# Performance work log

Hardware: AMD Instinct MI355X
Metric: run time of the kernel (lower is better)

Reference implementation:

```python
import jax, jax.numpy as jnp
import numpy as np


def poly_feature(x, degree):
    """Monomial feature expansion along channel dim, exactly matching the
    original index-tracking loop order. x: [B, n, H, W] -> [B, F, H, W]."""
    n = x.shape[1]
    feature = [x]
    index = list(range(n))
    for _d in range(1, degree):
        new = []
        k = 0
        for i in range(n):
            term = x[:, i:i + 1] * feature[-1][:, index[i]:]
            new.append(term)
            index[i] = k
            k = k + term.shape[1]
        feature.append(jnp.concatenate(new, axis=1))
    return jnp.concatenate(feature, axis=1)


def setup_inputs() -> dict:
    key = jax.random.key(0)
    k1, k2, k3 = jax.random.split(key, 3)
    B, C, H, W = 16, 3, 512, 512
    degree = 3
    F = 19  # monomials of degree 1..3 in 3 vars: 3 + 6 + 10
    x = jax.random.uniform(k1, (B, C, H, W), dtype=jnp.float32)
    weight = jax.random.normal(k2, (F, C), dtype=jnp.float32)
    bias = jax.random.normal(k3, (C,), dtype=jnp.float32)
    return {"x": x, "weight": weight, "bias": bias, "degree": degree}


def reference(x, weight, bias, degree):
    # f: [B, F, H, W]; linear map over feature dim -> [B, 3, H, W]
    f = poly_feature(x, degree)
    pred = jnp.einsum("bfhw,fc->bchw", f, weight) + bias[None, :, None, None]
    return pred
```

## Files before the change

### kernel.cpp

```cpp
#include <hip/hip_runtime.h>


constexpr int HW = 512 * 512;
constexpr int LOG2_HW = 18;

typedef float v4f __attribute__((ext_vector_type(4)));

__device__ __forceinline__ float rfl(float v) {
    return __uint_as_float(__builtin_amdgcn_readfirstlane(__float_as_uint(v)));
}

__global__ __launch_bounds__(256) void ct_kernel(
    const float* __restrict__ x, const float* __restrict__ wgt,
    const float* __restrict__ bias, float* __restrict__ out, int ngroups)
{
    float w[57];
#pragma unroll
    for (int i = 0; i < 57; ++i) w[i] = rfl(wgt[i]);
    const float b0 = rfl(bias[0]);
    const float b1 = rfl(bias[1]);
    const float b2 = rfl(bias[2]);

    const int g = blockIdx.x * blockDim.x + threadIdx.x;
    if (g >= ngroups) return;

    const int p  = g << 2;
    const int b  = p >> LOG2_HW;
    const int hw = p & (HW - 1);

    const float* base = x + (size_t)b * 3 * HW + hw;
    v4f v0 = __builtin_nontemporal_load(reinterpret_cast<const v4f*>(base));
    v4f v1 = __builtin_nontemporal_load(reinterpret_cast<const v4f*>(base + HW));
    v4f v2 = __builtin_nontemporal_load(reinterpret_cast<const v4f*>(base + 2 * HW));

    v4f o0, o1, o2;
#pragma unroll
    for (int j = 0; j < 4; ++j) {
        const float a = v0[j], bch = v1[j], c = v2[j];
        float f[19];
        f[0]  = a;          f[1]  = bch;        f[2]  = c;
        f[3]  = a * a;      f[4]  = a * bch;    f[5]  = a * c;
        f[6]  = bch * bch;  f[7]  = bch * c;    f[8]  = c * c;
        f[9]  = a * f[3];   f[10] = a * f[4];   f[11] = a * f[5];
        f[12] = a * f[6];   f[13] = a * f[7];   f[14] = a * f[8];
        f[15] = bch * f[6]; f[16] = bch * f[7]; f[17] = bch * f[8];
        f[18] = c * f[8];

        float s0 = b0, s1 = b1, s2 = b2;
#pragma unroll
        for (int k = 0; k < 19; ++k) {
            s0 = fmaf(f[k], w[3 * k + 0], s0);
            s1 = fmaf(f[k], w[3 * k + 1], s1);
            s2 = fmaf(f[k], w[3 * k + 2], s2);
        }
        o0[j] = s0; o1[j] = s1; o2[j] = s2;
    }

    float* obase = out + (size_t)b * 3 * HW + hw;
    __builtin_nontemporal_store(o0, reinterpret_cast<v4f*>(obase));
    __builtin_nontemporal_store(o1, reinterpret_cast<v4f*>(obase + HW));
    __builtin_nontemporal_store(o2, reinterpret_cast<v4f*>(obase + 2 * HW));
}

extern "C" void kernel_launch(void* const* d_in, const int* in_sizes, int n_in,
                              void* d_out, int out_size, void* d_ws, size_t ws_size,
                              hipStream_t stream) {
    const float* x    = (const float*)d_in[0];
    const float* wgt  = (const float*)d_in[1];
    const float* bias = (const float*)d_in[2];
    float* out = (float*)d_out;

    const int npix    = in_sizes[0] / 3;
    const int ngroups = npix / 4;
    const int block   = 256;
    const int grid    = (ngroups + block - 1) / block;
    ct_kernel<<<grid, block, 0, stream>>>(x, wgt, bias, out, ngroups);
}
```

Measured before the change: 24.13 us.

## Use grid-stride persistent loop with register prefetch of next group

Replaces the one-group-per-thread launch with a fixed grid of 1024 blocks that stride over all pixel groups, loading the next group's three channel vectors into registers before computing the current one. The goal is to overlap global-load latency with the polynomial FMAs and to amortise the weight and bias uniform loads across several groups. It also switches the nontemporal loads and stores to plain ones, which changes cache behaviour. The trade-offs are a fixed grid size and higher register pressure from the prefetched vectors.

```diff
diff --git a/kernel.cpp b/kernel.cpp
--- a/kernel.cpp
+++ b/kernel.cpp
@@ -8,6 +8,13 @@
 
 __device__ __forceinline__ float rfl(float v) {
     return __uint_as_float(__builtin_amdgcn_readfirstlane(__float_as_uint(v)));
+}
+
+__device__ __forceinline__ const float* group_base(const float* x, int g) {
+    const int p  = g << 2;
+    const int b  = p >> LOG2_HW;
+    const int hw = p & (HW - 1);
+    return x + (size_t)b * 3 * HW + hw;
 }
 
 __global__ __launch_bounds__(256) void ct_kernel(
@@ -21,45 +28,62 @@
     const float b1 = rfl(bias[1]);
     const float b2 = rfl(bias[2]);
 
-    const int g = blockIdx.x * blockDim.x + threadIdx.x;
+    const int nthreads = gridDim.x * blockDim.x;
+    int g = blockIdx.x * blockDim.x + threadIdx.x;
     if (g >= ngroups) return;
 
-    const int p  = g << 2;
-    const int b  = p >> LOG2_HW;
-    const int hw = p & (HW - 1);
+    const float* base = group_base(x, g);
+    v4f va = *reinterpret_cast<const v4f*>(base);
+    v4f vb = *reinterpret_cast<const v4f*>(base + HW);
+    v4f vc = *reinterpret_cast<const v4f*>(base + 2 * HW);
 
-    const float* base = x + (size_t)b * 3 * HW + hw;
-    v4f v0 = __builtin_nontemporal_load(reinterpret_cast<const v4f*>(base));
-    v4f v1 = __builtin_nontemporal_load(reinterpret_cast<const v4f*>(base + HW));
-    v4f v2 = __builtin_nontemporal_load(reinterpret_cast<const v4f*>(base + 2 * HW));
+    for (;;) {
+        const int gn = g + nthreads;
+        const bool has_next = gn < ngroups;
+        v4f na, nb, nc;
+        if (has_next) {
+            const float* nbase = group_base(x, gn);
+            na = *reinterpret_cast<const v4f*>(nbase);
+            nb = *reinterpret_cast<const v4f*>(nbase + HW);
+            nc = *reinterpret_cast<const v4f*>(nbase + 2 * HW);
+        }
 
-    v4f o0, o1, o2;
+        v4f o0, o1, o2;
 #pragma unroll
-    for (int j = 0; j < 4; ++j) {
-        const float a = v0[j], bch = v1[j], c = v2[j];
-        float f[19];
-        f[0]  = a;          f[1]  = bch;        f[2]  = c;
-        f[3]  = a * a;      f[4]  = a * bch;    f[5]  = a * c;
-        f[6]  = bch * bch;  f[7]  = bch * c;    f[8]  = c * c;
-        f[9]  = a * f[3];   f[10] = a * f[4];   f[11] = a * f[5];
-        f[12] = a * f[6];   f[13] = a * f[7];   f[14] = a * f[8];
-        f[15] = bch * f[6]; f[16] = bch * f[7]; f[17] = bch * f[8];
-        f[18] = c * f[8];
+        for (int j = 0; j < 4; ++j) {
+            const float a = va[j], bch = vb[j], c = vc[j];
+            float f[19];
+            f[0]  = a;          f[1]  = bch;        f[2]  = c;
+            f[3]  = a * a;      f[4]  = a * bch;    f[5]  = a * c;
+            f[6]  = bch * bch;  f[7]  = bch * c;    f[8]  = c * c;
+            f[9]  = a * f[3];   f[10] = a * f[4];   f[11] = a * f[5];
+            f[12] = a * f[6];   f[13] = a * f[7];   f[14] = a * f[8];
+            f[15] = bch * f[6]; f[16] = bch * f[7]; f[17] = bch * f[8];
+            f[18] = c * f[8];
 
-        float s0 = b0, s1 = b1, s2 = b2;
+            float s0 = b0, s1 = b1, s2 = b2;
 #pragma unroll
-        for (int k = 0; k < 19; ++k) {
-            s0 = fmaf(f[k], w[3 * k + 0], s0);
-            s1 = fmaf(f[k], w[3 * k + 1], s1);
-            s2 = fmaf(f[k], w[3 * k + 2], s2);
+            for (int k = 0; k < 19; ++k) {
+                s0 = fmaf(f[k], w[3 * k + 0], s0);
+                s1 = fmaf(f[k], w[3 * k + 1], s1);
+                s2 = fmaf(f[k], w[3 * k + 2], s2);
+            }
+            o0[j] = s0; o1[j] = s1; o2[j] = s2;
         }
-        o0[j] = s0; o1[j] = s1; o2[j] = s2;
+
+        {
+            const int p  = g << 2;
+            const int b  = p >> LOG2_HW;
+            const int hw = p & (HW - 1);
+            float* obase = out + (size_t)b * 3 * HW + hw;
+            *reinterpret_cast<v4f*>(obase)          = o0;
+            *reinterpret_cast<v4f*>(obase + HW)     = o1;
+            *reinterpret_cast<v4f*>(obase + 2 * HW) = o2;
+        }
+
+        if (!has_next) break;
+        va = na; vb = nb; vc = nc; g = gn;
     }
-
-    float* obase = out + (size_t)b * 3 * HW + hw;
-    __builtin_nontemporal_store(o0, reinterpret_cast<v4f*>(obase));
-    __builtin_nontemporal_store(o1, reinterpret_cast<v4f*>(obase + HW));
-    __builtin_nontemporal_store(o2, reinterpret_cast<v4f*>(obase + 2 * HW));
 }
 
 extern "C" void kernel_launch(void* const* d_in, const int* in_sizes, int n_in,
@@ -73,6 +97,6 @@
     const int npix    = in_sizes[0] / 3;
     const int ngroups = npix / 4;
     const int block   = 256;
-    const int grid    = (ngroups + block - 1) / block;
+    const int grid    = 1024;
     ct_kernel<<<grid, block, 0, stream>>>(x, wgt, bias, out, ngroups);
 }
```

After: 24.98 us. 1.04x slower.
